# Optimization experiments

Hardware: AMD Instinct MI355X
Metric: run time of the kernel (lower is better)

The kernel has to match this reference:

```python
import jax, jax.numpy as jnp
import numpy as np

B, S, D, H = 2, 2048, 768, 12
DH = D // H  # 64

def setup_inputs() -> dict:
    key = jax.random.key(0)
    ks = jax.random.split(key, 5)
    x = jax.random.normal(ks[0], (B, S, D), dtype=jnp.float32)
    # causal mask: True = attend (lower triangular), bool -> constant w.r.t. grads
    attn_mask = jnp.tril(jnp.ones((S, S), dtype=bool))[None, None, :, :]
    c_attn_w = jax.random.normal(ks[1], (D, 3 * D), dtype=jnp.float32) * 0.02
    c_attn_b = jnp.zeros((3 * D,), dtype=jnp.float32)
    c_proj_w = jax.random.normal(ks[2], (D, D), dtype=jnp.float32) * 0.02
    c_proj_b = jnp.zeros((D,), dtype=jnp.float32)
    return {"x": x, "attn_mask": attn_mask, "c_attn_w": c_attn_w,
            "c_attn_b": c_attn_b, "c_proj_w": c_proj_w, "c_proj_b": c_proj_b}

def reference(x, attn_mask, c_attn_w, c_attn_b, c_proj_w, c_proj_b):
    # qkv projection (Conv1D == addmm)
    qkv = x @ c_attn_w + c_attn_b                      # [B,S,3D]
    q, k, v = jnp.split(qkv, 3, axis=-1)               # each [B,S,D]
    def split_heads(t):
        return t.reshape(B, S, H, DH).transpose(0, 2, 1, 3)  # [B,H,S,DH]
    q, k, v = split_heads(q), split_heads(k), split_heads(v)
    scores = jnp.einsum('bhqd,bhkd->bhqk', q, k) / jnp.sqrt(jnp.float32(DH))
    neg = jnp.asarray(-1e9, dtype=scores.dtype)
    scores = jnp.where(attn_mask, scores, neg)         # additive causal mask
    probs = jax.nn.softmax(scores, axis=-1)            # dropout: eval mode (identity)
    out = jnp.einsum('bhqk,bhkd->bhqd', probs, v)      # [B,H,S,DH]
    out = out.transpose(0, 2, 1, 3).reshape(B, S, D)   # merge heads
    return out @ c_proj_w + c_proj_b
```

## Files before the change

### kernel.cpp

```cpp
#include <hip/hip_runtime.h>
#include <cstddef>
#include <cstdint>

#define Bsz  2
#define Ssz  2048
#define Dsz  768
#define Hsz  12
#define DHsz 64
#define Msz  4096
#define N3sz 2304
#define Kdim 768

typedef short bf16x8 __attribute__((ext_vector_type(8)));
typedef short bf16x4 __attribute__((ext_vector_type(4)));
typedef float f32x4  __attribute__((ext_vector_type(4)));
typedef const __attribute__((address_space(1))) void gvoid;
typedef __attribute__((address_space(3))) void lvoid;

static __device__ __forceinline__ unsigned short f2bf(float f) {
    unsigned int u = __builtin_bit_cast(unsigned int, f);
    u += 0x7FFFu + ((u >> 16) & 1u);
    return (unsigned short)(u >> 16);
}
static __device__ __forceinline__ unsigned int pk2bf(float a, float b) {
    return (unsigned int)f2bf(a) | ((unsigned int)f2bf(b) << 16);
}

static __device__ __forceinline__ void transpose_body(
    const float* __restrict__ W, unsigned short* __restrict__ Wt, int N,
    int bx, int by, int tid, float (*T)[65])
{
    const int n0 = bx << 6;
    const int k0 = by << 6;
#pragma unroll
    for (int p = 0; p < 4; ++p) {
        const int idx = p * 256 + tid;
        const int r  = idx >> 4;
        const int c4 = (idx & 15) << 2;
        const float4 v = *(const float4*)&W[(size_t)(k0 + r) * N + n0 + c4];
        T[r][c4 + 0] = v.x; T[r][c4 + 1] = v.y;
        T[r][c4 + 2] = v.z; T[r][c4 + 3] = v.w;
    }
    __syncthreads();
#pragma unroll
    for (int p = 0; p < 4; ++p) {
        const int idx = p * 256 + tid;
        const int r  = idx >> 4;
        const int c4 = (idx & 15) << 2;
        ushort4 o;
        o.x = f2bf(T[c4 + 0][r]); o.y = f2bf(T[c4 + 1][r]);
        o.z = f2bf(T[c4 + 2][r]); o.w = f2bf(T[c4 + 3][r]);
        *(ushort4*)&Wt[(size_t)(n0 + r) * Kdim + k0 + c4] = o;
    }
}

__global__ __launch_bounds__(256) void prep_kernel(
    const float* __restrict__ X, unsigned short* __restrict__ Xb,
    const float* __restrict__ Wqkv, unsigned short* __restrict__ Wqkvt,
    const float* __restrict__ Wproj, unsigned short* __restrict__ Wprojt)
{
    __shared__ float T[64][65];
    const int bid = blockIdx.x;
    const int tid = threadIdx.x;
    if (bid < 1536) {
        const size_t i = ((size_t)bid * 256 + tid) * 8;
        const float4 a = *(const float4*)&X[i];
        const float4 b = *(const float4*)&X[i + 4];
        ushort4 lo, hi;
        lo.x = f2bf(a.x); lo.y = f2bf(a.y); lo.z = f2bf(a.z); lo.w = f2bf(a.w);
        hi.x = f2bf(b.x); hi.y = f2bf(b.y); hi.z = f2bf(b.z); hi.w = f2bf(b.w);
        *(ushort4*)&Xb[i] = lo;
        *(ushort4*)&Xb[i + 4] = hi;
    } else if (bid < 1536 + 432) {
        const int idx = bid - 1536;
        transpose_body(Wqkv, Wqkvt, N3sz, idx % 36, idx / 36, tid, T);
    } else {
        const int idx = bid - 1968;
        transpose_body(Wproj, Wprojt, Dsz, idx % 12, idx / 12, tid, T);
    }
}

__global__ __launch_bounds__(256) void qkv_gemm_kernel(
    const unsigned short* __restrict__ A,
    const unsigned short* __restrict__ Bt,
    const float* __restrict__ bias,
    unsigned short* __restrict__ Qo, unsigned short* __restrict__ Ko,
    unsigned short* __restrict__ Vt)
{
    __shared__ unsigned short smem[128 * 136];
    unsigned short* Als = smem;
    unsigned short* Bls = smem + 8192;

    const int tid  = threadIdx.x;
    const int w    = tid >> 6;
    const int lane = tid & 63;
    const int quad = lane >> 4;
    const int t16  = lane & 15;
    const int wm   = w & 1;
    const int wn   = w >> 1;
    const int m0   = blockIdx.y << 7;
    const int n0   = blockIdx.x << 7;

    const int lrow = lane >> 3;
    const int lch  = lane & 7;
    const unsigned short* Ag = A  + (size_t)(m0 + lrow) * Kdim + ((lch ^ lrow) << 3);
    const unsigned short* Bg = Bt + (size_t)(n0 + lrow) * Kdim + ((lch ^ lrow) << 3);

    f32x4 acc[4][4];
#pragma unroll
    for (int mt = 0; mt < 4; ++mt)
#pragma unroll
        for (int nt = 0; nt < 4; ++nt) acc[mt][nt] = (f32x4)(0.f);

    for (int k0 = 0; k0 < Kdim; k0 += 64) {
        __syncthreads();
#pragma unroll
        for (int t = 0; t < 4; ++t) {
            const int i = (w << 2) + t;
            __builtin_amdgcn_global_load_lds(
                (gvoid*)(Ag + (size_t)(i << 3) * Kdim + k0),
                (lvoid*)(Als + (i << 9)), 16, 0, 0);
            __builtin_amdgcn_global_load_lds(
                (gvoid*)(Bg + (size_t)(i << 3) * Kdim + k0),
                (lvoid*)(Bls + (i << 9)), 16, 0, 0);
        }
        __syncthreads();

#pragma unroll
        for (int ks = 0; ks < 2; ++ks) {
            const int sl = (((ks << 2) + quad) ^ (t16 & 7)) << 3;
            bf16x8 af[4], bfr[4];
#pragma unroll
            for (int mt = 0; mt < 4; ++mt)
                af[mt] = *(const bf16x8*)&Als[(((wm << 6) + (mt << 4) + t16) << 6) + sl];
#pragma unroll
            for (int nt = 0; nt < 4; ++nt)
                bfr[nt] = *(const bf16x8*)&Bls[(((wn << 6) + (nt << 4) + t16) << 6) + sl];
#pragma unroll
            for (int mt = 0; mt < 4; ++mt)
#pragma unroll
                for (int nt = 0; nt < 4; ++nt)
                    acc[mt][nt] = __builtin_amdgcn_mfma_f32_16x16x32_bf16(
                        bfr[nt], af[mt], acc[mt][nt], 0, 0, 0);
        }
    }

    __syncthreads();
    {
        const int seg = n0 / Dsz;
        const float sc = (seg == 0) ? 0.18033688f : 1.0f;
#pragma unroll
        for (int nt = 0; nt < 4; ++nt) {
            const int nl = (wn << 6) + (nt << 4) + (quad << 2);
            const float4 bn = *(const float4*)&bias[n0 + nl];
#pragma unroll
            for (int mt = 0; mt < 4; ++mt) {
                const int ml = (wm << 6) + (mt << 4) + t16;
                uint2 o;
                o.x = pk2bf((acc[mt][nt][0] + bn.x) * sc,
                            (acc[mt][nt][1] + bn.y) * sc);
                o.y = pk2bf((acc[mt][nt][2] + bn.z) * sc,
                            (acc[mt][nt][3] + bn.w) * sc);
                *(uint2*)&smem[ml * 136 + nl] = o;
            }
        }
        __syncthreads();

        const int h0 = (n0 % Dsz) >> 6;
        const int bI = m0 >> 11;
        const int s0 = m0 & 2047;
        if (seg < 2) {
            unsigned short* dst0 = (seg == 0) ? Qo : Ko;
            const int chunk = tid & 7;
#pragma unroll
            for (int p = 0; p < 8; ++p) {
                const int unit = p * 32 + (tid >> 3);
                const int ml = unit >> 1;
                const int hc = unit & 1;
                const int s  = s0 + ml;
                const uint4 v = *(const uint4*)&smem[ml * 136 + (hc << 6) + (chunk << 3)];
                *(uint4*)&dst0[(((size_t)bI * Hsz + h0 + hc) * Ssz + s) * DHsz
                               + (chunk << 3)] = v;
            }
        } else {
            const int nrow = tid >> 1;
            const int mh   = tid & 1;
            const int d    = nrow & 63;
            const int hc   = nrow >> 6;
            unsigned short* dst = Vt
                + ((size_t)(bI * Hsz + h0 + hc) * DHsz + d) * Ssz + s0 + (mh << 6);
#pragma unroll
            for (int c = 0; c < 4; ++c) {
                unsigned int dw[8];
#pragma unroll
                for (int k = 0; k < 8; ++k) {
                    const int j = c * 16 + 2 * k;
                    dw[k] = (unsigned int)smem[((mh << 6) + j) * 136 + nrow]
                          | ((unsigned int)smem[((mh << 6) + j + 1) * 136 + nrow] << 16);
                }
                *(uint4*)&dst[c * 16]     = make_uint4(dw[0], dw[1], dw[2], dw[3]);
                *(uint4*)&dst[c * 16 + 8] = make_uint4(dw[4], dw[5], dw[6], dw[7]);
            }
        }
    }
}

__global__ __launch_bounds__(256) void proj_gemm_kernel(
    const unsigned short* __restrict__ A,
    const unsigned short* __restrict__ Bt,
    const float* __restrict__ bias, float* __restrict__ Out)
{
    __shared__ float smemf[64 * 68];
    unsigned short* Als = (unsigned short*)smemf;
    unsigned short* Bls = Als + 4096;

    const int tid  = threadIdx.x;
    const int w    = tid >> 6;
    const int lane = tid & 63;
    const int quad = lane >> 4;
    const int t16  = lane & 15;
    const int wm   = w & 1;
    const int wn   = w >> 1;
    const int m0   = blockIdx.y << 6;
    const int n0   = blockIdx.x << 6;

    const int lrow = lane >> 3;
    const int lch  = lane & 7;
    const unsigned short* Ag = A  + (size_t)(m0 + lrow) * Kdim + ((lch ^ lrow) << 3);
    const unsigned short* Bg = Bt + (size_t)(n0 + lrow) * Kdim + ((lch ^ lrow) << 3);

    f32x4 acc[2][2];
#pragma unroll
    for (int mt = 0; mt < 2; ++mt)
#pragma unroll
        for (int nt = 0; nt < 2; ++nt) acc[mt][nt] = (f32x4)(0.f);

    for (int k0 = 0; k0 < Kdim; k0 += 64) {
        __syncthreads();
#pragma unroll
        for (int t = 0; t < 2; ++t) {
            const int i = (w << 1) + t;
            __builtin_amdgcn_global_load_lds(
                (gvoid*)(Ag + (size_t)(i << 3) * Kdim + k0),
                (lvoid*)(Als + (i << 9)), 16, 0, 0);
            __builtin_amdgcn_global_load_lds(
                (gvoid*)(Bg + (size_t)(i << 3) * Kdim + k0),
                (lvoid*)(Bls + (i << 9)), 16, 0, 0);
        }
        __syncthreads();

#pragma unroll
        for (int ks = 0; ks < 2; ++ks) {
            const int sl = (((ks << 2) + quad) ^ (t16 & 7)) << 3;
            bf16x8 af[2], bfr[2];
#pragma unroll
            for (int mt = 0; mt < 2; ++mt)
                af[mt] = *(const bf16x8*)&Als[(((wm << 5) + (mt << 4) + t16) << 6) + sl];
#pragma unroll
            for (int nt = 0; nt < 2; ++nt)
                bfr[nt] = *(const bf16x8*)&Bls[(((wn << 5) + (nt << 4) + t16) << 6) + sl];
#pragma unroll
            for (int mt = 0; mt < 2; ++mt)
#pragma unroll
                for (int nt = 0; nt < 2; ++nt)
                    acc[mt][nt] = __builtin_amdgcn_mfma_f32_16x16x32_bf16(
                        bfr[nt], af[mt], acc[mt][nt], 0, 0, 0);
        }
    }

    __syncthreads();
#pragma unroll
    for (int nt = 0; nt < 2; ++nt) {
        const int nl = (wn << 5) + (nt << 4) + (quad << 2);
        const float4 bn = *(const float4*)&bias[n0 + nl];
#pragma unroll
        for (int mt = 0; mt < 2; ++mt) {
            const int ml = (wm << 5) + (mt << 4) + t16;
            float4 o;
            o.x = acc[mt][nt][0] + bn.x;
            o.y = acc[mt][nt][1] + bn.y;
            o.z = acc[mt][nt][2] + bn.z;
            o.w = acc[mt][nt][3] + bn.w;
            *(float4*)&smemf[ml * 68 + nl] = o;
        }
    }
    __syncthreads();
    {
        const int c16 = tid & 15;
#pragma unroll
        for (int p = 0; p < 4; ++p) {
            const int ml = p * 16 + (tid >> 4);
            const float4 v = *(const float4*)&smemf[ml * 68 + (c16 << 2)];
            *(float4*)&Out[(size_t)(m0 + ml) * Dsz + n0 + (c16 << 2)] = v;
        }
    }
}

__global__ __launch_bounds__(256) void attn_mfma_kernel(
    const unsigned short* __restrict__ Q, const unsigned short* __restrict__ K,
    const unsigned short* __restrict__ Vt, unsigned short* __restrict__ Aout)
{
    __shared__ unsigned short Kls[2][64 * 72];
    __shared__ unsigned short Vls[2][64 * 72];

    const int tid  = threadIdx.x;
    const int w    = tid >> 6;
    const int lane = tid & 63;
    const int quad = lane >> 4;
    const int t16  = lane & 15;

    const int c    = blockIdx.x & 255;
    const int slot = blockIdx.x >> 8;
    const int u    = (slot == 0) ? c : (slot == 1) ? (511 - c) : (512 + c);
    const int qt   = 31 - (u / 24);
    const int bh   = u % 24;
    const int q0   = qt << 6;
    const int bIdx = bh / Hsz;
    const int h    = bh % Hsz;

    const size_t base  = (size_t)bh * Ssz * DHsz;
    const size_t vbase = (size_t)bh * DHsz * Ssz;

    const int row_a = tid >> 3;
    const int ch_a  = tid & 7;

    bf16x8 qf[2];
#pragma unroll
    for (int s = 0; s < 2; ++s)
        qf[s] = *(const bf16x8*)&Q[base + (size_t)(q0 + w * 16 + t16) * DHsz
                                   + s * 32 + quad * 8];

    f32x4 O[4];
    float l_ps = 0.f;
#pragma unroll
    for (int dt = 0; dt < 4; ++dt) O[dt] = (f32x4)(0.f);

    {
        const unsigned short* Kb = K + base;
        const unsigned short* Vb = Vt + vbase;
        const uint4 k0a = *(const uint4*)&Kb[(size_t)row_a * DHsz + ch_a * 8];
        const uint4 k0b = *(const uint4*)&Kb[(size_t)(row_a + 32) * DHsz + ch_a * 8];
        const uint4 v0a = *(const uint4*)&Vb[(size_t)row_a * Ssz + ch_a * 8];
        const uint4 v0b = *(const uint4*)&Vb[(size_t)(row_a + 32) * Ssz + ch_a * 8];
        *(uint4*)&Kls[0][row_a * 72 + ch_a * 8] = k0a;
        *(uint4*)&Kls[0][(row_a + 32) * 72 + ch_a * 8] = k0b;
        *(uint4*)&Vls[0][row_a * 72 + ch_a * 8] = v0a;
        *(uint4*)&Vls[0][(row_a + 32) * 72 + ch_a * 8] = v0b;
    }
    __syncthreads();

    for (int kt = 0; kt <= qt; ++kt) {
        const int cur = kt & 1;
        const int nxt = cur ^ 1;

        uint4 kr0, kr1, vr0, vr1;
        if (kt < qt) {
            const unsigned short* Kb = K + base + (size_t)((kt + 1) << 6) * DHsz;
            const unsigned short* Vb = Vt + vbase + ((kt + 1) << 6);
            kr0 = *(const uint4*)&Kb[(size_t)row_a * DHsz + ch_a * 8];
            kr1 = *(const uint4*)&Kb[(size_t)(row_a + 32) * DHsz + ch_a * 8];
            vr0 = *(const uint4*)&Vb[(size_t)row_a * Ssz + ch_a * 8];
            vr1 = *(const uint4*)&Vb[(size_t)(row_a + 32) * Ssz + ch_a * 8];
        }

        f32x4 St[4];
#pragma unroll
        for (int kb = 0; kb < 4; ++kb) St[kb] = (f32x4)(0.f);
#pragma unroll
        for (int s = 0; s < 2; ++s)
#pragma unroll
            for (int kb = 0; kb < 4; ++kb) {
                const bf16x8 kf = *(const bf16x8*)&Kls[cur][(kb * 16 + t16) * 72
                                                           + s * 32 + quad * 8];
                St[kb] = __builtin_amdgcn_mfma_f32_16x16x32_bf16(kf, qf[s], St[kb], 0, 0, 0);
            }

        if (kt == qt) {
            const int qrel = w * 16 + t16;
#pragma unroll
            for (int kb = 0; kb < 4; ++kb) {
                const int kvb = kb * 16 + quad * 4;
#pragma unroll
                for (int r = 0; r < 4; ++r)
                    if (kvb + r > qrel) St[kb][r] = -1e30f;
            }
        }

#pragma unroll
        for (int kb = 0; kb < 4; ++kb) {
            const float p0 = exp2f(St[kb][0]);
            const float p1 = exp2f(St[kb][1]);
            const float p2 = exp2f(St[kb][2]);
            const float p3 = exp2f(St[kb][3]);
            l_ps += (p0 + p1) + (p2 + p3);
            uint2 pk;
            pk.x = pk2bf(p0, p1);
            pk.y = pk2bf(p2, p3);
            const bf16x4 pf = __builtin_bit_cast(bf16x4, pk);
#pragma unroll
            for (int dt = 0; dt < 4; ++dt) {
                const bf16x4 vf = *(const bf16x4*)&Vls[cur][(dt * 16 + t16) * 72
                                                            + kb * 16 + quad * 4];
                O[dt] = __builtin_amdgcn_mfma_f32_16x16x16bf16_1k(vf, pf, O[dt], 0, 0, 0);
            }
        }

        if (kt < qt) {
            *(uint4*)&Kls[nxt][row_a * 72 + ch_a * 8] = kr0;
            *(uint4*)&Kls[nxt][(row_a + 32) * 72 + ch_a * 8] = kr1;
            *(uint4*)&Vls[nxt][row_a * 72 + ch_a * 8] = vr0;
            *(uint4*)&Vls[nxt][(row_a + 32) * 72 + ch_a * 8] = vr1;
            __syncthreads();
        }
    }

    l_ps += __shfl_xor(l_ps, 16);
    l_ps += __shfl_xor(l_ps, 32);
    {
        const float inv = 1.0f / l_ps;
        const int q = q0 + w * 16 + t16;
        unsigned short* dst = Aout + ((size_t)bIdx * Ssz + q) * Dsz + (h << 6);
#pragma unroll
        for (int dt = 0; dt < 4; ++dt) {
            uint2 o;
            o.x = pk2bf(O[dt][0] * inv, O[dt][1] * inv);
            o.y = pk2bf(O[dt][2] * inv, O[dt][3] * inv);
            *(uint2*)&dst[dt * 16 + quad * 4] = o;
        }
    }
}

extern "C" void kernel_launch(void* const* d_in, const int* in_sizes, int n_in,
                              void* d_out, int out_size, void* d_ws, size_t ws_size,
                              hipStream_t stream) {
    const float* x        = (const float*)d_in[0];
    const float* c_attn_w = (const float*)d_in[2];
    const float* c_attn_b = (const float*)d_in[3];
    const float* c_proj_w = (const float*)d_in[4];
    const float* c_proj_b = (const float*)d_in[5];
    float* out = (float*)d_out;

    const size_t T = (size_t)Msz * Dsz;
    unsigned short* xb     = (unsigned short*)d_ws;
    unsigned short* Wqkvt  = xb + T;
    unsigned short* Wprojt = Wqkvt + (size_t)N3sz * Kdim;
    unsigned short* Qw     = Wprojt + (size_t)Dsz * Kdim;
    unsigned short* Kw     = Qw + T;
    unsigned short* Vw     = Kw + T;
    unsigned short* Ab     = Vw + T;

    prep_kernel<<<2112, 256, 0, stream>>>(x, xb, c_attn_w, Wqkvt, c_proj_w, Wprojt);
    qkv_gemm_kernel<<<dim3(N3sz / 128, Msz / 128), 256, 0, stream>>>(
        xb, Wqkvt, c_attn_b, Qw, Kw, Vw);
    attn_mfma_kernel<<<32 * 24, 256, 0, stream>>>(Qw, Kw, Vw, Ab);
    proj_gemm_kernel<<<dim3(Dsz / 64, Msz / 64), 256, 0, stream>>>(
        Ab, Wprojt, c_proj_b, out);
}
```

Measured before the change: 164.3 us.

## Use persistent attention blocks with an atomic work queue for causal tiles

The attention kernel changes from a fixed grid of 768 blocks with a hand-built tile order to 512 persistent blocks. Each block repeatedly takes the next (query tile, head) item from a global atomic counter, longest causal tiles first. The counter is reset inside the prep kernel. The goal is better load balance across CUs for uneven causal work, at the cost of an atomic and two barriers per item and fewer blocks resident at once.

```diff
diff --git a/kernel.cpp b/kernel.cpp
--- a/kernel.cpp
+++ b/kernel.cpp
@@ -57,11 +57,13 @@
 __global__ __launch_bounds__(256) void prep_kernel(
     const float* __restrict__ X, unsigned short* __restrict__ Xb,
     const float* __restrict__ Wqkv, unsigned short* __restrict__ Wqkvt,
-    const float* __restrict__ Wproj, unsigned short* __restrict__ Wprojt)
+    const float* __restrict__ Wproj, unsigned short* __restrict__ Wprojt,
+    unsigned int* __restrict__ counter)
 {
     __shared__ float T[64][65];
     const int bid = blockIdx.x;
     const int tid = threadIdx.x;
+    if (bid == 0 && tid == 0) *counter = 0;
     if (bid < 1536) {
         const size_t i = ((size_t)bid * 256 + tid) * 8;
         const float4 a = *(const float4*)&X[i];
@@ -298,10 +300,12 @@
 
 __global__ __launch_bounds__(256) void attn_mfma_kernel(
     const unsigned short* __restrict__ Q, const unsigned short* __restrict__ K,
-    const unsigned short* __restrict__ Vt, unsigned short* __restrict__ Aout)
+    const unsigned short* __restrict__ Vt, unsigned short* __restrict__ Aout,
+    unsigned int* __restrict__ counter)
 {
     __shared__ unsigned short Kls[2][64 * 72];
     __shared__ unsigned short Vls[2][64 * 72];
+    __shared__ unsigned int s_item;
 
     const int tid  = threadIdx.x;
     const int w    = tid >> 6;
@@ -309,123 +313,129 @@
     const int quad = lane >> 4;
     const int t16  = lane & 15;
 
-    const int c    = blockIdx.x & 255;
-    const int slot = blockIdx.x >> 8;
-    const int u    = (slot == 0) ? c : (slot == 1) ? (511 - c) : (512 + c);
-    const int qt   = 31 - (u / 24);
-    const int bh   = u % 24;
-    const int q0   = qt << 6;
-    const int bIdx = bh / Hsz;
-    const int h    = bh % Hsz;
-
-    const size_t base  = (size_t)bh * Ssz * DHsz;
-    const size_t vbase = (size_t)bh * DHsz * Ssz;
-
     const int row_a = tid >> 3;
     const int ch_a  = tid & 7;
 
-    bf16x8 qf[2];
-#pragma unroll
-    for (int s = 0; s < 2; ++s)
-        qf[s] = *(const bf16x8*)&Q[base + (size_t)(q0 + w * 16 + t16) * DHsz
-                                   + s * 32 + quad * 8];
-
-    f32x4 O[4];
-    float l_ps = 0.f;
-#pragma unroll
-    for (int dt = 0; dt < 4; ++dt) O[dt] = (f32x4)(0.f);
-
-    {
-        const unsigned short* Kb = K + base;
-        const unsigned short* Vb = Vt + vbase;
-        const uint4 k0a = *(const uint4*)&Kb[(size_t)row_a * DHsz + ch_a * 8];
-        const uint4 k0b = *(const uint4*)&Kb[(size_t)(row_a + 32) * DHsz + ch_a * 8];
-        const uint4 v0a = *(const uint4*)&Vb[(size_t)row_a * Ssz + ch_a * 8];
-        const uint4 v0b = *(const uint4*)&Vb[(size_t)(row_a + 32) * Ssz + ch_a * 8];
-        *(uint4*)&Kls[0][row_a * 72 + ch_a * 8] = k0a;
-        *(uint4*)&Kls[0][(row_a + 32) * 72 + ch_a * 8] = k0b;
-        *(uint4*)&Vls[0][row_a * 72 + ch_a * 8] = v0a;
-        *(uint4*)&Vls[0][(row_a + 32) * 72 + ch_a * 8] = v0b;
-    }
-    __syncthreads();
-
-    for (int kt = 0; kt <= qt; ++kt) {
-        const int cur = kt & 1;
-        const int nxt = cur ^ 1;
-
-        uint4 kr0, kr1, vr0, vr1;
-        if (kt < qt) {
-            const unsigned short* Kb = K + base + (size_t)((kt + 1) << 6) * DHsz;
-            const unsigned short* Vb = Vt + vbase + ((kt + 1) << 6);
-            kr0 = *(const uint4*)&Kb[(size_t)row_a * DHsz + ch_a * 8];
-            kr1 = *(const uint4*)&Kb[(size_t)(row_a + 32) * DHsz + ch_a * 8];
-            vr0 = *(const uint4*)&Vb[(size_t)row_a * Ssz + ch_a * 8];
-            vr1 = *(const uint4*)&Vb[(size_t)(row_a + 32) * Ssz + ch_a * 8];
-        }
-
-        f32x4 St[4];
-#pragma unroll
-        for (int kb = 0; kb < 4; ++kb) St[kb] = (f32x4)(0.f);
+    for (;;) {
+        __syncthreads();
+        if (tid == 0) s_item = atomicAdd(counter, 1u);
+        __syncthreads();
+        const unsigned int u = s_item;
+        if (u >= 768u) break;
+
+        const int qt   = 31 - (int)(u / 24);
+        const int bh   = (int)(u % 24);
+        const int q0   = qt << 6;
+        const int bIdx = bh / Hsz;
+        const int h    = bh % Hsz;
+
+        const size_t base  = (size_t)bh * Ssz * DHsz;
+        const size_t vbase = (size_t)bh * DHsz * Ssz;
+
+        bf16x8 qf[2];
 #pragma unroll
         for (int s = 0; s < 2; ++s)
+            qf[s] = *(const bf16x8*)&Q[base + (size_t)(q0 + w * 16 + t16) * DHsz
+                                       + s * 32 + quad * 8];
+
+        f32x4 O[4];
+        float l_ps = 0.f;
+#pragma unroll
+        for (int dt = 0; dt < 4; ++dt) O[dt] = (f32x4)(0.f);
+
+        {
+            const unsigned short* Kb = K + base;
+            const unsigned short* Vb = Vt + vbase;
+            const uint4 k0a = *(const uint4*)&Kb[(size_t)row_a * DHsz + ch_a * 8];
+            const uint4 k0b = *(const uint4*)&Kb[(size_t)(row_a + 32) * DHsz + ch_a * 8];
+            const uint4 v0a = *(const uint4*)&Vb[(size_t)row_a * Ssz + ch_a * 8];
+            const uint4 v0b = *(const uint4*)&Vb[(size_t)(row_a + 32) * Ssz + ch_a * 8];
+            *(uint4*)&Kls[0][row_a * 72 + ch_a * 8] = k0a;
+            *(uint4*)&Kls[0][(row_a + 32) * 72 + ch_a * 8] = k0b;
+            *(uint4*)&Vls[0][row_a * 72 + ch_a * 8] = v0a;
+            *(uint4*)&Vls[0][(row_a + 32) * 72 + ch_a * 8] = v0b;
+        }
+        __syncthreads();
+
+        for (int kt = 0; kt <= qt; ++kt) {
+            const int cur = kt & 1;
+            const int nxt = cur ^ 1;
+
+            uint4 kr0, kr1, vr0, vr1;
+            if (kt < qt) {
+                const unsigned short* Kb = K + base + (size_t)((kt + 1) << 6) * DHsz;
+                const unsigned short* Vb = Vt + vbase + ((kt + 1) << 6);
+                kr0 = *(const uint4*)&Kb[(size_t)row_a * DHsz + ch_a * 8];
+                kr1 = *(const uint4*)&Kb[(size_t)(row_a + 32) * DHsz + ch_a * 8];
+                vr0 = *(const uint4*)&Vb[(size_t)row_a * Ssz + ch_a * 8];
+                vr1 = *(const uint4*)&Vb[(size_t)(row_a + 32) * Ssz + ch_a * 8];
+            }
+
+            f32x4 St[4];
+#pragma unroll
+            for (int kb = 0; kb < 4; ++kb) St[kb] = (f32x4)(0.f);
+#pragma unroll
+            for (int s = 0; s < 2; ++s)
+#pragma unroll
+                for (int kb = 0; kb < 4; ++kb) {
+                    const bf16x8 kf = *(const bf16x8*)&Kls[cur][(kb * 16 + t16) * 72
+                                                               + s * 32 + quad * 8];
+                    St[kb] = __builtin_amdgcn_mfma_f32_16x16x32_bf16(
+                        kf, qf[s], St[kb], 0, 0, 0);
+                }
+
+            if (kt == qt) {
+                const int qrel = w * 16 + t16;
+#pragma unroll
+                for (int kb = 0; kb < 4; ++kb) {
+                    const int kvb = kb * 16 + quad * 4;
+#pragma unroll
+                    for (int r = 0; r < 4; ++r)
+                        if (kvb + r > qrel) St[kb][r] = -1e30f;
+                }
+            }
+
 #pragma unroll
             for (int kb = 0; kb < 4; ++kb) {
-                const bf16x8 kf = *(const bf16x8*)&Kls[cur][(kb * 16 + t16) * 72
-                                                           + s * 32 + quad * 8];
-                St[kb] = __builtin_amdgcn_mfma_f32_16x16x32_bf16(kf, qf[s], St[kb], 0, 0, 0);
-            }
-
-        if (kt == qt) {
-            const int qrel = w * 16 + t16;
-#pragma unroll
-            for (int kb = 0; kb < 4; ++kb) {
-                const int kvb = kb * 16 + quad * 4;
-#pragma unroll
-                for (int r = 0; r < 4; ++r)
-                    if (kvb + r > qrel) St[kb][r] = -1e30f;
-            }
-        }
-
-#pragma unroll
-        for (int kb = 0; kb < 4; ++kb) {
-            const float p0 = exp2f(St[kb][0]);
-            const float p1 = exp2f(St[kb][1]);
-            const float p2 = exp2f(St[kb][2]);
-            const float p3 = exp2f(St[kb][3]);
-            l_ps += (p0 + p1) + (p2 + p3);
-            uint2 pk;
-            pk.x = pk2bf(p0, p1);
-            pk.y = pk2bf(p2, p3);
-            const bf16x4 pf = __builtin_bit_cast(bf16x4, pk);
+                const float p0 = exp2f(St[kb][0]);
+                const float p1 = exp2f(St[kb][1]);
+                const float p2 = exp2f(St[kb][2]);
+                const float p3 = exp2f(St[kb][3]);
+                l_ps += (p0 + p1) + (p2 + p3);
+                uint2 pk;
+                pk.x = pk2bf(p0, p1);
+                pk.y = pk2bf(p2, p3);
+                const bf16x4 pf = __builtin_bit_cast(bf16x4, pk);
+#pragma unroll
+                for (int dt = 0; dt < 4; ++dt) {
+                    const bf16x4 vf = *(const bf16x4*)&Vls[cur][(dt * 16 + t16) * 72
+                                                                + kb * 16 + quad * 4];
+                    O[dt] = __builtin_amdgcn_mfma_f32_16x16x16bf16_1k(vf, pf, O[dt], 0, 0, 0);
+                }
+            }
+
+            if (kt < qt) {
+                *(uint4*)&Kls[nxt][row_a * 72 + ch_a * 8] = kr0;
+                *(uint4*)&Kls[nxt][(row_a + 32) * 72 + ch_a * 8] = kr1;
+                *(uint4*)&Vls[nxt][row_a * 72 + ch_a * 8] = vr0;
+                *(uint4*)&Vls[nxt][(row_a + 32) * 72 + ch_a * 8] = vr1;
+                __syncthreads();
+            }
+        }
+
+        l_ps += __shfl_xor(l_ps, 16);
+        l_ps += __shfl_xor(l_ps, 32);
+        {
+            const float inv = 1.0f / l_ps;
+            const int q = q0 + w * 16 + t16;
+            unsigned short* dst = Aout + ((size_t)bIdx * Ssz + q) * Dsz + (h << 6);
 #pragma unroll
             for (int dt = 0; dt < 4; ++dt) {
-                const bf16x4 vf = *(const bf16x4*)&Vls[cur][(dt * 16 + t16) * 72
-                                                            + kb * 16 + quad * 4];
-                O[dt] = __builtin_amdgcn_mfma_f32_16x16x16bf16_1k(vf, pf, O[dt], 0, 0, 0);
-            }
-        }
-
-        if (kt < qt) {
-            *(uint4*)&Kls[nxt][row_a * 72 + ch_a * 8] = kr0;
-            *(uint4*)&Kls[nxt][(row_a + 32) * 72 + ch_a * 8] = kr1;
-            *(uint4*)&Vls[nxt][row_a * 72 + ch_a * 8] = vr0;
-            *(uint4*)&Vls[nxt][(row_a + 32) * 72 + ch_a * 8] = vr1;
-            __syncthreads();
-        }
-    }
-
-    l_ps += __shfl_xor(l_ps, 16);
-    l_ps += __shfl_xor(l_ps, 32);
-    {
-        const float inv = 1.0f / l_ps;
-        const int q = q0 + w * 16 + t16;
-        unsigned short* dst = Aout + ((size_t)bIdx * Ssz + q) * Dsz + (h << 6);
-#pragma unroll
-        for (int dt = 0; dt < 4; ++dt) {
-            uint2 o;
-            o.x = pk2bf(O[dt][0] * inv, O[dt][1] * inv);
-            o.y = pk2bf(O[dt][2] * inv, O[dt][3] * inv);
-            *(uint2*)&dst[dt * 16 + quad * 4] = o;
+                uint2 o;
+                o.x = pk2bf(O[dt][0] * inv, O[dt][1] * inv);
+                o.y = pk2bf(O[dt][2] * inv, O[dt][3] * inv);
+                *(uint2*)&dst[dt * 16 + quad * 4] = o;
+            }
         }
     }
 }
@@ -448,11 +458,13 @@
     unsigned short* Kw     = Qw + T;
     unsigned short* Vw     = Kw + T;
     unsigned short* Ab     = Vw + T;
-
-    prep_kernel<<<2112, 256, 0, stream>>>(x, xb, c_attn_w, Wqkvt, c_proj_w, Wprojt);
+    unsigned int*   cnt    = (unsigned int*)(Ab + T);
+
+    prep_kernel<<<2112, 256, 0, stream>>>(x, xb, c_attn_w, Wqkvt,
+                                          c_proj_w, Wprojt, cnt);
     qkv_gemm_kernel<<<dim3(N3sz / 128, Msz / 128), 256, 0, stream>>>(
         xb, Wqkvt, c_attn_b, Qw, Kw, Vw);
-    attn_mfma_kernel<<<32 * 24, 256, 0, stream>>>(Qw, Kw, Vw, Ab);
+    attn_mfma_kernel<<<512, 256, 0, stream>>>(Qw, Kw, Vw, Ab, cnt);
     proj_gemm_kernel<<<dim3(Dsz / 64, Msz / 64), 256, 0, stream>>>(
         Ab, Wprojt, c_proj_b, out);
 }
```

Result: slower. 172.3 us (+4.9%).
